# Performance work log

Hardware: AMD Instinct MI355X
Metric: run time of the kernel (lower is better)

Reference implementation:

```python
import jax, jax.numpy as jnp
import numpy as np

EMBED_DIM = 1024
NUM_HEADS = 16
HEAD_DIM = EMBED_DIM // NUM_HEADS
B, S = 2, 2048


def setup_inputs() -> dict:
    key = jax.random.key(0)
    ks = jax.random.split(key, 11)
    f32 = jnp.float32
    return {
        "q": jax.random.normal(ks[0], (B, S, EMBED_DIM), f32),
        "k": jax.random.normal(ks[1], (B, S, EMBED_DIM), f32),
        "v": jax.random.normal(ks[2], (B, S, EMBED_DIM), f32),
        # per-head projection weights stacked over heads: [H, E, Dh]
        "Wq": jax.random.normal(ks[3], (NUM_HEADS, EMBED_DIM, HEAD_DIM), f32),
        "Wk": jax.random.normal(ks[4], (NUM_HEADS, EMBED_DIM, HEAD_DIM), f32),
        "Wv": jax.random.normal(ks[5], (NUM_HEADS, EMBED_DIM, HEAD_DIM), f32),
        "bq": jax.random.normal(ks[6], (NUM_HEADS, HEAD_DIM), f32),
        "bk": jax.random.normal(ks[7], (NUM_HEADS, HEAD_DIM), f32),
        "bv": jax.random.normal(ks[8], (NUM_HEADS, HEAD_DIM), f32),
        "Wo": jax.random.normal(ks[9], (EMBED_DIM, EMBED_DIM), f32),
        "bo": jax.random.normal(ks[10], (EMBED_DIM,), f32),
    }


def reference(q, k, v, Wq, Wk, Wv, bq, bk, bv, Wo, bo):
    scale = jnp.asarray(np.sqrt(HEAD_DIM), q.dtype)
    # batched per-head projections: [B,S,E] x [H,E,D] -> [B,H,S,D]
    Q = jnp.einsum("bse,hed->bhsd", q, Wq) + bq[None, :, None, :]
    K = jnp.einsum("bse,hed->bhsd", k, Wk) + bk[None, :, None, :]
    V = jnp.einsum("bse,hed->bhsd", v, Wv) + bv[None, :, None, :]
    # attention scores [B,H,S,S]; original applies mask to a discarded tensor,
    # so output is unmasked softmax(QK^T/scale) @ V
    att = jnp.einsum("bhsd,bhtd->bhst", Q, K) / scale
    att = jax.nn.softmax(att, axis=-1)
    ctx = jnp.einsum("bhst,bhtd->bhsd", att, V)  # [B,H,S,D]
    # concat heads (head order preserved) then output projection
    ctx = ctx.transpose(0, 2, 1, 3).reshape(ctx.shape[0], ctx.shape[2], -1)  # [B,S,E]
    return ctx @ Wo + bo
```

## Files before the change

### kernel.cpp

```cpp
#include <hip/hip_runtime.h>
#include <hip/hip_bf16.h>

typedef unsigned short u16;
typedef unsigned int   u32;
typedef _Float16 f16;
typedef __attribute__((ext_vector_type(4))) float f32x4;
typedef __attribute__((ext_vector_type(8))) short s16x8;
typedef __attribute__((ext_vector_type(8))) f16 f16x8;
typedef __attribute__((ext_vector_type(2))) __fp16 fp16x2;
typedef __attribute__((ext_vector_type(4))) u16 u16x4;
typedef __attribute__((ext_vector_type(2))) u32 u32x2;

#define DI __device__ __forceinline__

static constexpr int Bb = 2, Ss = 2048, Hh = 16, Dd = 64, Ee = 1024;
static constexpr int Mrows = Bb * Ss;
static constexpr size_t NE = (size_t)Mrows * Ee;
static constexpr size_t WN = (size_t)Ee * Ee;
static constexpr float QSCALE = 0.125f * 1.44269504088896f;

DI float bf2f(u16 h) { u32 u = ((u32)h) << 16; return __builtin_bit_cast(float, u); }
DI u16 f2bf(float f) {
    u32 u = __builtin_bit_cast(u32, f);
    u32 r = (u + 0x7FFFu + ((u >> 16) & 1u)) >> 16;
    return (u16)r;
}
DI u16 f2h(float f) { f16 h = (f16)f; return __builtin_bit_cast(u16, h); }
DI u32 pkrtz(float a, float b) {
    fp16x2 r = __builtin_amdgcn_cvt_pkrtz(a, b);
    return __builtin_bit_cast(u32, r);
}
DI float ex2(float x) { return __builtin_amdgcn_exp2f(x); }

#define MFMA_BF(a, b, c) __builtin_amdgcn_mfma_f32_16x16x32_bf16((a), (b), (c), 0, 0, 0)
#define MFMA_F16(a, b, c) __builtin_amdgcn_mfma_f32_16x16x32_f16( \
    __builtin_bit_cast(f16x8, (a)), __builtin_bit_cast(f16x8, (b)), (c), 0, 0, 0)

DI void gld16(const u16* g, u16* l) {
    __builtin_amdgcn_global_load_lds((const __attribute__((address_space(1))) void*)g,
                                     (__attribute__((address_space(3))) void*)l, 16, 0, 0);
}

__global__ __launch_bounds__(256) void k_split3(
    const float* __restrict__ q, const float* __restrict__ k, const float* __restrict__ v,
    u16* __restrict__ qh, u16* __restrict__ ql,
    u16* __restrict__ kh, u16* __restrict__ kl, u16* __restrict__ vh) {
    int i = blockIdx.x * 256 + threadIdx.x;
    int y = blockIdx.y;
    if (y == 2) { vh[i] = f2h(v[i]); return; }
    const float* s = y ? k : q;
    u16* h = y ? kh : qh;
    u16* l = y ? kl : ql;
    float val = s[i];
    u16 hh = f2bf(val);
    h[i] = hh;
    l[i] = f2bf(val - bf2f(hh));
}

__global__ __launch_bounds__(256) void k_wprep(
    const float* __restrict__ Wq, const float* __restrict__ Wk,
    const float* __restrict__ Wv, const float* __restrict__ Wo,
    u16* __restrict__ WqTh, u16* __restrict__ WqTl,
    u16* __restrict__ WkTh, u16* __restrict__ WkTl,
    u16* __restrict__ WvT, u16* __restrict__ WoT) {
    __shared__ float Ts[64 * 65];
    const int y = blockIdx.y;
    const int ti = blockIdx.x >> 4, tj = blockIdx.x & 15;
    const float* W = (y == 0) ? Wq : (y == 1) ? Wk : (y == 2) ? Wv : Wo;
    const int t = threadIdx.x;
    const int col = t & 63, rb = (t >> 6) * 16;
#pragma unroll
    for (int rr = 0; rr < 16; rr++) {
        int row = rb + rr;
        float v = (y < 3) ? W[(size_t)ti * 65536 + (size_t)(tj * 64 + row) * 64 + col]
                          : W[(size_t)(tj * 64 + row) * Ee + ti * 64 + col];
        Ts[row * 65 + col] = v;
    }
    __syncthreads();
#pragma unroll
    for (int rr = 0; rr < 16; rr++) {
        int orow = rb + rr;
        int ocol = col;
        float v = Ts[ocol * 65 + orow];
        size_t oidx = (size_t)(ti * 64 + orow) * Ee + tj * 64 + ocol;
        if (y == 0) {
            u16 hh = f2bf(v); WqTh[oidx] = hh; WqTl[oidx] = f2bf(v - bf2f(hh));
        } else if (y == 1) {
            u16 hh = f2bf(v); WkTh[oidx] = hh; WkTl[oidx] = f2bf(v - bf2f(hh));
        } else if (y == 2) {
            WvT[oidx] = f2h(v);
        } else {
            WoT[oidx] = f2h(v);
        }
    }
}

template <int SPLIT, int F16, int OUTMODE>
DI void gemm_body(const u16* __restrict__ Ah, const u16* __restrict__ Al,
                  const u16* __restrict__ Bh, const u16* __restrict__ Bl,
                  const float* __restrict__ bias,
                  u16* __restrict__ C16h, u16* __restrict__ C16l, float* __restrict__ Cf,
                  float scale, u16* As0, u16* As1, u16* Bs0, u16* Bs1) {
    constexpr int M = Mrows, N = Ee, K = Ee;
    const int tid = threadIdx.x;
    const int wave = tid >> 6, lane = tid & 63;
    const int quad = lane >> 4, l16 = lane & 15;
    const int m0 = blockIdx.y * 128, n0 = blockIdx.x * 128;
    const int wm = (wave >> 1) * 64, wn = (wave & 1) * 64;

    f32x4 acc[4][4];
#pragma unroll
    for (int i = 0; i < 4; i++)
#pragma unroll
        for (int j = 0; j < 4; j++) acc[i][j] = (f32x4)0.0f;

    for (int kk = 0; kk < K; kk += 32) {
        __syncthreads();
#pragma unroll
        for (int i = 0; i < 2; i++) {
            int c = tid + i * 256;
            int row = c >> 2, j = c & 3;
            size_t ga = (size_t)(m0 + row) * K + kk + j * 8;
            gld16(Ah + ga, As0 + c * 8);
            if constexpr (SPLIT) gld16(Al + ga, As1 + c * 8);
            size_t gb = (size_t)(n0 + row) * K + kk + j * 8;
            gld16(Bh + gb, Bs0 + c * 8);
            if constexpr (SPLIT) gld16(Bl + gb, Bs1 + c * 8);
        }
        __syncthreads();

        s16x8 bf[4][2];
#pragma unroll
        for (int nt = 0; nt < 4; nt++) {
            int r = wn + nt * 16 + l16;
            bf[nt][0] = *(const s16x8*)&Bs0[r * 32 + quad * 8];
            if constexpr (SPLIT) bf[nt][1] = *(const s16x8*)&Bs1[r * 32 + quad * 8];
        }
#pragma unroll
        for (int mt = 0; mt < 4; mt++) {
            int r = wm + mt * 16 + l16;
            s16x8 a0 = *(const s16x8*)&As0[r * 32 + quad * 8];
            s16x8 a1;
            if constexpr (SPLIT) a1 = *(const s16x8*)&As1[r * 32 + quad * 8];
#pragma unroll
            for (int nt = 0; nt < 4; nt++) {
                if constexpr (F16) {
                    acc[mt][nt] = MFMA_F16(a0, bf[nt][0], acc[mt][nt]);
                } else {
                    acc[mt][nt] = MFMA_BF(a0, bf[nt][0], acc[mt][nt]);
                    if constexpr (SPLIT) {
                        acc[mt][nt] = MFMA_BF(a0, bf[nt][1], acc[mt][nt]);
                        acc[mt][nt] = MFMA_BF(a1, bf[nt][0], acc[mt][nt]);
                    }
                }
            }
        }
    }

#pragma unroll
    for (int mt = 0; mt < 4; mt++)
#pragma unroll
        for (int nt = 0; nt < 4; nt++) {
            int gn = n0 + wn + nt * 16 + l16;
            float bs = bias[gn];
            if constexpr (OUTMODE == 1) {
                int gm = m0 + wm + mt * 16 + quad * 4;
                u16x4 pk;
#pragma unroll
                for (int r = 0; r < 4; r++) pk[r] = f2h((acc[mt][nt][r] + bs) * scale);
                *(u16x4*)&C16h[(size_t)gn * M + gm] = pk;
            } else {
#pragma unroll
                for (int r = 0; r < 4; r++) {
                    int gm = m0 + wm + mt * 16 + quad * 4 + r;
                    float v = (acc[mt][nt][r] + bs) * scale;
                    if constexpr (OUTMODE == 0) {
                        Cf[(size_t)gm * N + gn] = v;
                    } else {
                        u16 hh = f2bf(v);
                        C16h[(size_t)gm * N + gn] = hh;
                        C16l[(size_t)gm * N + gn] = f2bf(v - bf2f(hh));
                    }
                }
            }
        }
}

__global__ __launch_bounds__(256, 3) void k_qkv(
    const u16* __restrict__ qh, const u16* __restrict__ ql,
    const u16* __restrict__ kh, const u16* __restrict__ kl,
    const u16* __restrict__ vh,
    const u16* __restrict__ WqTh, const u16* __restrict__ WqTl,
    const u16* __restrict__ WkTh, const u16* __restrict__ WkTl,
    const u16* __restrict__ WvT,
    const float* __restrict__ bq, const float* __restrict__ bk, const float* __restrict__ bv,
    u16* __restrict__ Qh, u16* __restrict__ Ql2,
    u16* __restrict__ Kh, u16* __restrict__ Kl2, u16* __restrict__ Vt) {
    __shared__ u16 As[2][128 * 32];
    __shared__ u16 Bs[2][128 * 32];
    int z = blockIdx.z;
    if (z == 0)
        gemm_body<1, 0, 2>(qh, ql, WqTh, WqTl, bq, Qh, Ql2, nullptr, QSCALE,
                           As[0], As[1], Bs[0], Bs[1]);
    else if (z == 1)
        gemm_body<1, 0, 2>(kh, kl, WkTh, WkTl, bk, Kh, Kl2, nullptr, 1.0f,
                           As[0], As[1], Bs[0], Bs[1]);
    else
        gemm_body<0, 1, 1>(vh, nullptr, WvT, nullptr, bv, Vt, nullptr, nullptr, 1.0f,
                           As[0], As[1], Bs[0], Bs[1]);
}

__global__ __launch_bounds__(256, 3) void k_out(
    const u16* __restrict__ ctx, const u16* __restrict__ WoT,
    const float* __restrict__ bo, float* __restrict__ out) {
    __shared__ u16 As[128 * 32];
    __shared__ u16 Bs[128 * 32];
    gemm_body<0, 1, 0>(ctx, nullptr, WoT, nullptr, bo, nullptr, nullptr, out, 1.0f,
                       As, nullptr, Bs, nullptr);
}

__global__ __launch_bounds__(256, 2) void k_attn(
    const u16* __restrict__ Qh, const u16* __restrict__ Ql,
    const u16* __restrict__ Kh, const u16* __restrict__ Kl,
    const u16* __restrict__ Vt, u16* __restrict__ ctx) {
    const int bh = blockIdx.x;
    const int b = bh >> 4, h = bh & 15;
    const int q0 = blockIdx.y * 128;
    const int rowBase = b * Ss + q0;
    const int hc = h * 64;

    __shared__ u16 Ks[2][2][64 * 64];
    __shared__ u16 Vs[2][64 * 64];
    __shared__ u16 Pw[4][32 * 72];

    const int tid = threadIdx.x;
    const int wave = tid >> 6, lane = tid & 63;
    const int quad = lane >> 4, l16 = lane & 15;

    const int c0 = tid, c1 = tid + 256;
    const int srow0 = c0 >> 3, sj0 = (c0 & 7) ^ (srow0 & 7);
    const int srow1 = c1 >> 3, sj1 = (c1 & 7) ^ (srow1 & 7);

    auto stage = [&](int t0, int bf) {
        const size_t kb = (size_t)(b * Ss + t0) * Ee + hc;
        const size_t vb0 = (size_t)(hc + srow0) * Mrows + b * Ss + t0;
        const size_t vb1 = (size_t)(hc + srow1) * Mrows + b * Ss + t0;
        gld16(Kh + kb + (size_t)srow0 * Ee + sj0 * 8, &Ks[bf][0][c0 * 8]);
        gld16(Kh + kb + (size_t)srow1 * Ee + sj1 * 8, &Ks[bf][0][c1 * 8]);
        gld16(Kl + kb + (size_t)srow0 * Ee + sj0 * 8, &Ks[bf][1][c0 * 8]);
        gld16(Kl + kb + (size_t)srow1 * Ee + sj1 * 8, &Ks[bf][1][c1 * 8]);
        gld16(Vt + vb0 + sj0 * 8, &Vs[bf][c0 * 8]);
        gld16(Vt + vb1 + sj1 * 8, &Vs[bf][c1 * 8]);
    };

    const int sw0 = ((0 * 4 + quad) ^ (l16 & 7)) * 8;
    const int sw1 = ((1 * 4 + quad) ^ (l16 & 7)) * 8;
    const int kro0 = l16 * 64 + sw0;
    const int kro1 = l16 * 64 + sw1;
    u16* pwb = &Pw[wave][l16 * 72 + quad * 4];
    const u16* pbb = &Pw[wave][l16 * 72 + quad * 8];

    s16x8 bq[2][2][2];
#pragma unroll
    for (int nt = 0; nt < 2; nt++) {
        int row = rowBase + wave * 32 + nt * 16 + l16;
#pragma unroll
        for (int kc = 0; kc < 2; kc++) {
            bq[nt][kc][0] = *(const s16x8*)(Qh + (size_t)row * Ee + hc + kc * 32 + quad * 8);
            bq[nt][kc][1] = *(const s16x8*)(Ql + (size_t)row * Ee + hc + kc * 32 + quad * 8);
        }
    }

    f32x4 o[2][4];
#pragma unroll
    for (int nt = 0; nt < 2; nt++)
#pragma unroll
        for (int dg = 0; dg < 4; dg++) o[nt][dg] = (f32x4)0.0f;
    float m_[2] = {-1e30f, -1e30f};
    float l_[2] = {0.f, 0.f};

    stage(0, 0);
    __syncthreads();

    for (int t0 = 0; t0 < Ss; t0 += 64) {
        const int p = (t0 >> 6) & 1;
        if (t0 + 64 < Ss) stage(t0 + 64, p ^ 1);

        const u16* Kp = &Ks[p][0][0];
        const u16* Vp = &Vs[p][0];

        f32x4 st[2][4];
#pragma unroll
        for (int nt = 0; nt < 2; nt++)
#pragma unroll
            for (int mt = 0; mt < 4; mt++) st[nt][mt] = (f32x4)0.0f;
        __builtin_amdgcn_s_setprio(1);
#pragma unroll
        for (int mt = 0; mt < 4; mt++) {
            s16x8 akh0 = *(const s16x8*)(Kp + kro0 + mt * 1024);
            s16x8 akl0 = *(const s16x8*)(Kp + kro0 + mt * 1024 + 4096);
            s16x8 akh1 = *(const s16x8*)(Kp + kro1 + mt * 1024);
            s16x8 akl1 = *(const s16x8*)(Kp + kro1 + mt * 1024 + 4096);
#pragma unroll
            for (int nt = 0; nt < 2; nt++) {
                st[nt][mt] = MFMA_BF(akh0, bq[nt][0][0], st[nt][mt]);
                st[nt][mt] = MFMA_BF(akh0, bq[nt][0][1], st[nt][mt]);
                st[nt][mt] = MFMA_BF(akl0, bq[nt][0][0], st[nt][mt]);
                st[nt][mt] = MFMA_BF(akh1, bq[nt][1][0], st[nt][mt]);
                st[nt][mt] = MFMA_BF(akh1, bq[nt][1][1], st[nt][mt]);
                st[nt][mt] = MFMA_BF(akl1, bq[nt][1][0], st[nt][mt]);
            }
        }
        __builtin_amdgcn_s_setprio(0);

#pragma unroll
        for (int nt = 0; nt < 2; nt++) {
            float t01 = fmaxf(fmaxf(st[nt][0][0], st[nt][0][1]), fmaxf(st[nt][0][2], st[nt][0][3]));
            float t23 = fmaxf(fmaxf(st[nt][1][0], st[nt][1][1]), fmaxf(st[nt][1][2], st[nt][1][3]));
            float t45 = fmaxf(fmaxf(st[nt][2][0], st[nt][2][1]), fmaxf(st[nt][2][2], st[nt][2][3]));
            float t67 = fmaxf(fmaxf(st[nt][3][0], st[nt][3][1]), fmaxf(st[nt][3][2], st[nt][3][3]));
            float tmax = fmaxf(fmaxf(t01, t23), fmaxf(t45, t67));
            tmax = fmaxf(tmax, __shfl_xor(tmax, 16));
            tmax = fmaxf(tmax, __shfl_xor(tmax, 32));
            float mnew = fmaxf(m_[nt], tmax);
            float al = ex2(m_[nt] - mnew);
            m_[nt] = mnew;
            float psum = 0.f;
#pragma unroll
            for (int mt = 0; mt < 4; mt++) {
                float p0 = ex2(st[nt][mt][0] - mnew);
                float p1 = ex2(st[nt][mt][1] - mnew);
                float p2 = ex2(st[nt][mt][2] - mnew);
                float p3 = ex2(st[nt][mt][3] - mnew);
                psum += (p0 + p1) + (p2 + p3);
                u32x2 pk;
                pk[0] = pkrtz(p0, p1);
                pk[1] = pkrtz(p2, p3);
                *(u32x2*)(pwb + nt * 1152 + mt * 16) = pk;
            }
            psum += __shfl_xor(psum, 16);
            psum += __shfl_xor(psum, 32);
            l_[nt] = l_[nt] * al + psum;
#pragma unroll
            for (int dg = 0; dg < 4; dg++) o[nt][dg] *= al;
        }

        __builtin_amdgcn_s_setprio(1);
#pragma unroll
        for (int kc = 0; kc < 2; kc++) {
            s16x8 bp[2];
#pragma unroll
            for (int nt = 0; nt < 2; nt++)
                bp[nt] = *(const s16x8*)(pbb + nt * 1152 + kc * 32);
            const int vro = kc ? kro1 : kro0;
#pragma unroll
            for (int dg = 0; dg < 4; dg++) {
                s16x8 av = *(const s16x8*)(Vp + vro + dg * 1024);
#pragma unroll
                for (int nt = 0; nt < 2; nt++) o[nt][dg] = MFMA_F16(av, bp[nt], o[nt][dg]);
            }
        }
        __builtin_amdgcn_s_setprio(0);

        __syncthreads();
    }

#pragma unroll
    for (int nt = 0; nt < 2; nt++) {
        float inv = 1.0f / l_[nt];
        int gm = rowBase + wave * 32 + nt * 16 + l16;
#pragma unroll
        for (int dg = 0; dg < 4; dg++) {
            u32x2 pk;
            pk[0] = pkrtz(o[nt][dg][0] * inv, o[nt][dg][1] * inv);
            pk[1] = pkrtz(o[nt][dg][2] * inv, o[nt][dg][3] * inv);
            *(u32x2*)&ctx[(size_t)gm * Ee + hc + dg * 16 + quad * 4] = pk;
        }
    }
}

extern "C" void kernel_launch(void* const* d_in, const int* in_sizes, int n_in,
                              void* d_out, int out_size, void* d_ws, size_t ws_size,
                              hipStream_t stream) {
    const float* q   = (const float*)d_in[0];
    const float* kin = (const float*)d_in[1];
    const float* v   = (const float*)d_in[2];
    const float* Wq  = (const float*)d_in[3];
    const float* Wk  = (const float*)d_in[4];
    const float* Wv  = (const float*)d_in[5];
    const float* bq  = (const float*)d_in[6];
    const float* bk  = (const float*)d_in[7];
    const float* bv  = (const float*)d_in[8];
    const float* Wo  = (const float*)d_in[9];
    const float* bo  = (const float*)d_in[10];

    u16* ws = (u16*)d_ws;
    u16 *qh = ws,          *ql = ws + NE,     *kh = ws + 2 * NE, *kl = ws + 3 * NE;
    u16 *vh = ws + 4 * NE;
    u16 *Qh = ws + 5 * NE, *Ql = ws + 6 * NE, *Kh = ws + 7 * NE, *Kl = ws + 8 * NE;
    u16 *Vt = ws + 9 * NE, *ctx = ws + 10 * NE;
    u16 *WqTh = ws + 11 * NE;
    u16 *WqTl = WqTh + WN, *WkTh = WqTh + 2 * WN, *WkTl = WqTh + 3 * WN;
    u16 *WvT = WqTh + 4 * WN, *WoT = WqTh + 5 * WN;

    dim3 b256(256);
    k_split3<<<dim3(NE / 256, 3), b256, 0, stream>>>(q, kin, v, qh, ql, kh, kl, vh);
    k_wprep<<<dim3(256, 4), b256, 0, stream>>>(Wq, Wk, Wv, Wo,
                                               WqTh, WqTl, WkTh, WkTl, WvT, WoT);

    k_qkv<<<dim3(8, 32, 3), b256, 0, stream>>>(qh, ql, kh, kl, vh,
                                               WqTh, WqTl, WkTh, WkTl, WvT,
                                               bq, bk, bv, Qh, Ql, Kh, Kl, Vt);

    k_attn<<<dim3(Bb * Hh, Ss / 128), b256, 0, stream>>>(Qh, Ql, Kh, Kl, Vt, ctx);

    k_out<<<dim3(8, 32), b256, 0, stream>>>(ctx, WoT, bo, (float*)d_out);
}
```

Baseline: 299.6 us.

## Switch attention to 32x32x16 MFMA and keep P in registers via permlane32 swap

Rewrites the attention inner loop to use 32x32x16 MFMA tiles for both QK^T and PV instead of 16x16x32, so each wave owns 32 query rows with a single softmax state per lane. The P matrix is repacked in registers using permlane32_swap instead of going through a per-wave LDS scratch buffer, which removes that LDS buffer and its write/read round trip. The larger tiles reduce the number of MFMA issues and K/V LDS reads per tile, but raise accumulator register pressure and depend on the lane-layout mapping being correct.

```diff
diff --git a/kernel.cpp b/kernel.cpp
--- a/kernel.cpp
+++ b/kernel.cpp
@@ -5,11 +5,13 @@
 typedef unsigned int   u32;
 typedef _Float16 f16;
 typedef __attribute__((ext_vector_type(4))) float f32x4;
+typedef __attribute__((ext_vector_type(16))) float f32x16;
 typedef __attribute__((ext_vector_type(8))) short s16x8;
 typedef __attribute__((ext_vector_type(8))) f16 f16x8;
 typedef __attribute__((ext_vector_type(2))) __fp16 fp16x2;
 typedef __attribute__((ext_vector_type(4))) u16 u16x4;
 typedef __attribute__((ext_vector_type(2))) u32 u32x2;
+typedef __attribute__((ext_vector_type(4))) u32 u32x4;
 
 #define DI __device__ __forceinline__
 
@@ -34,6 +36,9 @@
 
 #define MFMA_BF(a, b, c) __builtin_amdgcn_mfma_f32_16x16x32_bf16((a), (b), (c), 0, 0, 0)
 #define MFMA_F16(a, b, c) __builtin_amdgcn_mfma_f32_16x16x32_f16( \
+    __builtin_bit_cast(f16x8, (a)), __builtin_bit_cast(f16x8, (b)), (c), 0, 0, 0)
+#define MFMA32_BF(a, b, c) __builtin_amdgcn_mfma_f32_32x32x16_bf16((a), (b), (c), 0, 0, 0)
+#define MFMA32_F16(a, b, c) __builtin_amdgcn_mfma_f32_32x32x16_f16( \
     __builtin_bit_cast(f16x8, (a)), __builtin_bit_cast(f16x8, (b)), (c), 0, 0, 0)
 
 DI void gld16(const u16* g, u16* l) {
@@ -231,11 +236,11 @@
 
     __shared__ u16 Ks[2][2][64 * 64];
     __shared__ u16 Vs[2][64 * 64];
-    __shared__ u16 Pw[4][32 * 72];
 
     const int tid = threadIdx.x;
     const int wave = tid >> 6, lane = tid & 63;
-    const int quad = lane >> 4, l16 = lane & 15;
+    const int l31 = lane & 31, hi = lane >> 5;
+    const int swl = l31 & 7;
 
     const int c0 = tid, c1 = tid + 256;
     const int srow0 = c0 >> 3, sj0 = (c0 & 7) ^ (srow0 & 7);
@@ -253,31 +258,20 @@
         gld16(Vt + vb1 + sj1 * 8, &Vs[bf][c1 * 8]);
     };
 
-    const int sw0 = ((0 * 4 + quad) ^ (l16 & 7)) * 8;
-    const int sw1 = ((1 * 4 + quad) ^ (l16 & 7)) * 8;
-    const int kro0 = l16 * 64 + sw0;
-    const int kro1 = l16 * 64 + sw1;
-    u16* pwb = &Pw[wave][l16 * 72 + quad * 4];
-    const u16* pbb = &Pw[wave][l16 * 72 + quad * 8];
-
-    s16x8 bq[2][2][2];
-#pragma unroll
-    for (int nt = 0; nt < 2; nt++) {
-        int row = rowBase + wave * 32 + nt * 16 + l16;
-#pragma unroll
-        for (int kc = 0; kc < 2; kc++) {
-            bq[nt][kc][0] = *(const s16x8*)(Qh + (size_t)row * Ee + hc + kc * 32 + quad * 8);
-            bq[nt][kc][1] = *(const s16x8*)(Ql + (size_t)row * Ee + hc + kc * 32 + quad * 8);
+    s16x8 bqh[4], bql[4];
+    {
+        const size_t qoff = (size_t)(rowBase + wave * 32 + l31) * Ee + hc + hi * 8;
+#pragma unroll
+        for (int ks = 0; ks < 4; ks++) {
+            bqh[ks] = *(const s16x8*)(Qh + qoff + ks * 16);
+            bql[ks] = *(const s16x8*)(Ql + qoff + ks * 16);
         }
     }
 
-    f32x4 o[2][4];
-#pragma unroll
-    for (int nt = 0; nt < 2; nt++)
-#pragma unroll
-        for (int dg = 0; dg < 4; dg++) o[nt][dg] = (f32x4)0.0f;
-    float m_[2] = {-1e30f, -1e30f};
-    float l_[2] = {0.f, 0.f};
+    f32x16 o[2];
+    o[0] = (f32x16)0.0f;
+    o[1] = (f32x16)0.0f;
+    float m_ = -1e30f, l_ = 0.f;
 
     stage(0, 0);
     __syncthreads();
@@ -289,75 +283,73 @@
         const u16* Kp = &Ks[p][0][0];
         const u16* Vp = &Vs[p][0];
 
-        f32x4 st[2][4];
-#pragma unroll
-        for (int nt = 0; nt < 2; nt++)
-#pragma unroll
-            for (int mt = 0; mt < 4; mt++) st[nt][mt] = (f32x4)0.0f;
+        f32x16 st[2];
+        st[0] = (f32x16)0.0f;
+        st[1] = (f32x16)0.0f;
         __builtin_amdgcn_s_setprio(1);
 #pragma unroll
-        for (int mt = 0; mt < 4; mt++) {
-            s16x8 akh0 = *(const s16x8*)(Kp + kro0 + mt * 1024);
-            s16x8 akl0 = *(const s16x8*)(Kp + kro0 + mt * 1024 + 4096);
-            s16x8 akh1 = *(const s16x8*)(Kp + kro1 + mt * 1024);
-            s16x8 akl1 = *(const s16x8*)(Kp + kro1 + mt * 1024 + 4096);
-#pragma unroll
-            for (int nt = 0; nt < 2; nt++) {
-                st[nt][mt] = MFMA_BF(akh0, bq[nt][0][0], st[nt][mt]);
-                st[nt][mt] = MFMA_BF(akh0, bq[nt][0][1], st[nt][mt]);
-                st[nt][mt] = MFMA_BF(akl0, bq[nt][0][0], st[nt][mt]);
-                st[nt][mt] = MFMA_BF(akh1, bq[nt][1][0], st[nt][mt]);
-                st[nt][mt] = MFMA_BF(akh1, bq[nt][1][1], st[nt][mt]);
-                st[nt][mt] = MFMA_BF(akl1, bq[nt][1][0], st[nt][mt]);
+        for (int mt = 0; mt < 2; mt++) {
+            const int rb = (mt * 32 + l31) * 64;
+#pragma unroll
+            for (int ks = 0; ks < 4; ks++) {
+                const int sj = ((2 * ks + hi) ^ swl) * 8;
+                s16x8 akh = *(const s16x8*)(Kp + rb + sj);
+                s16x8 akl = *(const s16x8*)(Kp + rb + sj + 4096);
+                st[mt] = MFMA32_BF(akh, bqh[ks], st[mt]);
+                st[mt] = MFMA32_BF(akh, bql[ks], st[mt]);
+                st[mt] = MFMA32_BF(akl, bqh[ks], st[mt]);
             }
         }
         __builtin_amdgcn_s_setprio(0);
 
-#pragma unroll
-        for (int nt = 0; nt < 2; nt++) {
-            float t01 = fmaxf(fmaxf(st[nt][0][0], st[nt][0][1]), fmaxf(st[nt][0][2], st[nt][0][3]));
-            float t23 = fmaxf(fmaxf(st[nt][1][0], st[nt][1][1]), fmaxf(st[nt][1][2], st[nt][1][3]));
-            float t45 = fmaxf(fmaxf(st[nt][2][0], st[nt][2][1]), fmaxf(st[nt][2][2], st[nt][2][3]));
-            float t67 = fmaxf(fmaxf(st[nt][3][0], st[nt][3][1]), fmaxf(st[nt][3][2], st[nt][3][3]));
-            float tmax = fmaxf(fmaxf(t01, t23), fmaxf(t45, t67));
-            tmax = fmaxf(tmax, __shfl_xor(tmax, 16));
-            tmax = fmaxf(tmax, __shfl_xor(tmax, 32));
-            float mnew = fmaxf(m_[nt], tmax);
-            float al = ex2(m_[nt] - mnew);
-            m_[nt] = mnew;
-            float psum = 0.f;
-#pragma unroll
-            for (int mt = 0; mt < 4; mt++) {
-                float p0 = ex2(st[nt][mt][0] - mnew);
-                float p1 = ex2(st[nt][mt][1] - mnew);
-                float p2 = ex2(st[nt][mt][2] - mnew);
-                float p3 = ex2(st[nt][mt][3] - mnew);
-                psum += (p0 + p1) + (p2 + p3);
-                u32x2 pk;
-                pk[0] = pkrtz(p0, p1);
-                pk[1] = pkrtz(p2, p3);
-                *(u32x2*)(pwb + nt * 1152 + mt * 16) = pk;
+        float tmax = st[0][0];
+#pragma unroll
+        for (int mt = 0; mt < 2; mt++)
+#pragma unroll
+            for (int r = 0; r < 16; r++) tmax = fmaxf(tmax, st[mt][r]);
+        tmax = fmaxf(tmax, __shfl_xor(tmax, 32));
+        float mnew = fmaxf(m_, tmax);
+        float al = ex2(m_ - mnew);
+        m_ = mnew;
+        float psum = 0.f;
+#pragma unroll
+        for (int mt = 0; mt < 2; mt++)
+#pragma unroll
+            for (int r = 0; r < 16; r++) {
+                st[mt][r] = ex2(st[mt][r] - mnew);
+                psum += st[mt][r];
             }
-            psum += __shfl_xor(psum, 16);
-            psum += __shfl_xor(psum, 32);
-            l_[nt] = l_[nt] * al + psum;
-#pragma unroll
-            for (int dg = 0; dg < 4; dg++) o[nt][dg] *= al;
+        psum += __shfl_xor(psum, 32);
+        l_ = l_ * al + psum;
+        o[0] *= al;
+        o[1] *= al;
+
+        s16x8 pa[4];
+#pragma unroll
+        for (int kt = 0; kt < 4; kt++) {
+            const int G0 = 2 * kt, G1 = 2 * kt + 1;
+            const int m0_ = G0 >> 2, r0_ = (G0 & 3) * 4;
+            const int m1_ = G1 >> 2, r1_ = (G1 & 3) * 4;
+            u32 wA0 = pkrtz(st[m0_][r0_ + 0], st[m0_][r0_ + 1]);
+            u32 wB0 = pkrtz(st[m0_][r0_ + 2], st[m0_][r0_ + 3]);
+            u32 wA1 = pkrtz(st[m1_][r1_ + 0], st[m1_][r1_ + 1]);
+            u32 wB1 = pkrtz(st[m1_][r1_ + 2], st[m1_][r1_ + 3]);
+            u32x2 rA = __builtin_amdgcn_permlane32_swap(wA0, wA1, false, false);
+            u32x2 rB = __builtin_amdgcn_permlane32_swap(wB0, wB1, false, false);
+            u32x4 w;
+            w[0] = rA[0]; w[1] = rB[0]; w[2] = rA[1]; w[3] = rB[1];
+            pa[kt] = __builtin_bit_cast(s16x8, w);
         }
 
         __builtin_amdgcn_s_setprio(1);
 #pragma unroll
-        for (int kc = 0; kc < 2; kc++) {
-            s16x8 bp[2];
-#pragma unroll
-            for (int nt = 0; nt < 2; nt++)
-                bp[nt] = *(const s16x8*)(pbb + nt * 1152 + kc * 32);
-            const int vro = kc ? kro1 : kro0;
-#pragma unroll
-            for (int dg = 0; dg < 4; dg++) {
-                s16x8 av = *(const s16x8*)(Vp + vro + dg * 1024);
-#pragma unroll
-                for (int nt = 0; nt < 2; nt++) o[nt][dg] = MFMA_F16(av, bp[nt], o[nt][dg]);
+        for (int dt = 0; dt < 2; dt++) {
+            const int rbv = (dt * 32 + l31) * 64;
+#pragma unroll
+            for (int kt = 0; kt < 4; kt++) {
+                const int sj = ((2 * kt + hi) ^ swl) * 8;
+                s16x8 av = *(const s16x8*)(Vp + rbv + sj);
+                o[dt] = MFMA32_F16(av, pa[kt], o[dt]);
             }
         }
         __builtin_amdgcn_s_setprio(0);
@@ -365,18 +357,17 @@
         __syncthreads();
     }
 
-#pragma unroll
-    for (int nt = 0; nt < 2; nt++) {
-        float inv = 1.0f / l_[nt];
-        int gm = rowBase + wave * 32 + nt * 16 + l16;
-#pragma unroll
-        for (int dg = 0; dg < 4; dg++) {
+    float inv = 1.0f / l_;
+    const size_t obase = (size_t)(rowBase + wave * 32 + l31) * Ee + hc + hi * 4;
+#pragma unroll
+    for (int dt = 0; dt < 2; dt++)
+#pragma unroll
+        for (int g = 0; g < 4; g++) {
             u32x2 pk;
-            pk[0] = pkrtz(o[nt][dg][0] * inv, o[nt][dg][1] * inv);
-            pk[1] = pkrtz(o[nt][dg][2] * inv, o[nt][dg][3] * inv);
-            *(u32x2*)&ctx[(size_t)gm * Ee + hc + dg * 16 + quad * 4] = pk;
-        }
-    }
+            pk[0] = pkrtz(o[dt][g * 4 + 0] * inv, o[dt][g * 4 + 1] * inv);
+            pk[1] = pkrtz(o[dt][g * 4 + 2] * inv, o[dt][g * 4 + 3] * inv);
+            *(u32x2*)&ctx[obase + dt * 32 + g * 8] = pk;
+        }
 }
 
 extern "C" void kernel_launch(void* const* d_in, const int* in_sizes, int n_in,
```

Result: no change. 294.4 us (-1.8%).
